# Optimization experiments

Measured on AMD Instinct MI355X. Metric: run time of the kernel, lower is better.

The kernel has to match this reference:

```python
import jax, jax.numpy as jnp
import numpy as np

PST_THD = 0.05
NMS_THD = 0.5
TOP_K = 1000  # max candidates kept before greedy NMS (fixed for jit)
IMG = 1024
NUM_CLASSES = 80


def _make_anchors(H, W):
    # Standard RetinaNet anchors: P3-P7, 3 ratios x 3 scales = 9 per location.
    levels = [3, 4, 5, 6, 7]
    ratios = np.array([0.5, 1.0, 2.0])
    scales = np.array([2 ** 0, 2 ** (1.0 / 3.0), 2 ** (2.0 / 3.0)])
    all_a = []
    for l in levels:
        stride = 2 ** l
        size = 2 ** (l + 2)
        base = []
        for r in ratios:
            for s in scales:
                area = (size * s) ** 2
                w = np.sqrt(area / r)
                h = w * r
                base.append([-w / 2, -h / 2, w / 2, h / 2])
        base = np.asarray(base)  # (9,4)
        fh, fw = H // stride, W // stride
        sx = (np.arange(fw) + 0.5) * stride
        sy = (np.arange(fh) + 0.5) * stride
        sxx, syy = np.meshgrid(sx, sy)
        shifts = np.stack([sxx.ravel(), syy.ravel(), sxx.ravel(), syy.ravel()], 1)
        all_a.append((shifts[:, None, :] + base[None, :, :]).reshape(-1, 4))
    return np.concatenate(all_a, 0).astype(np.float32)  # (A,4)


def setup_inputs() -> dict:
    key = jax.random.key(0)
    k1, k2 = jax.random.split(key)
    anchors = jnp.asarray(_make_anchors(IMG, IMG))  # (A,4)
    A = anchors.shape[0]
    classification = jax.random.uniform(k1, (1, A, NUM_CLASSES), dtype=jnp.float32)
    regression = jax.random.normal(k2, (1, A, 4), dtype=jnp.float32) * 0.5
    return {
        "classification": classification,
        "regression": regression,
        "anchors": anchors,
        "height": IMG,
        "width": IMG,
    }


def _postprocess(classification, regression, anchors, height, width):
    cls = classification[0]   # (A,C)
    reg = regression[0]       # (A,4)
    # --- BBoxTransform (std = [0.1,0.1,0.2,0.2]) ---
    wa = anchors[:, 2] - anchors[:, 0]
    ha = anchors[:, 3] - anchors[:, 1]
    cxa = anchors[:, 0] + 0.5 * wa
    cya = anchors[:, 1] + 0.5 * ha
    pcx = cxa + reg[:, 0] * 0.1 * wa
    pcy = cya + reg[:, 1] * 0.1 * ha
    pw = jnp.exp(reg[:, 2] * 0.2) * wa
    ph = jnp.exp(reg[:, 3] * 0.2) * ha
    # --- ClipBoxes ---
    x1 = jnp.clip(pcx - 0.5 * pw, 0.0, None)
    y1 = jnp.clip(pcy - 0.5 * ph, 0.0, None)
    x2 = jnp.minimum(pcx + 0.5 * pw, jnp.float32(width))
    y2 = jnp.minimum(pcy + 0.5 * ph, jnp.float32(height))
    boxes = jnp.stack([x1, y1, x2, y2], axis=1)  # (A,4)
    # --- score threshold + top-K candidate selection ---
    scores = jnp.max(cls, axis=1)
    class_id = jnp.argmax(cls, axis=1).astype(jnp.int32)
    masked = jnp.where(scores > PST_THD, scores, -1.0)
    top_s, idx = jax.lax.top_k(masked, TOP_K)  # sorted descending
    b = boxes[idx]                             # (K,4)
    c = class_id[idx]
    valid = top_s > PST_THD
    # --- greedy NMS over K candidates (classic py_cpu_nms, +1 areas) ---
    area = (b[:, 2] - b[:, 0] + 1.0) * (b[:, 3] - b[:, 1] + 1.0)
    xx1 = jnp.maximum(b[:, None, 0], b[None, :, 0])
    yy1 = jnp.maximum(b[:, None, 1], b[None, :, 1])
    xx2 = jnp.minimum(b[:, None, 2], b[None, :, 2])
    yy2 = jnp.minimum(b[:, None, 3], b[None, :, 3])
    inter = jnp.clip(xx2 - xx1 + 1.0, 0.0) * jnp.clip(yy2 - yy1 + 1.0, 0.0)
    iou = inter / (area[:, None] + area[None, :] - inter)  # (K,K)
    later = jnp.arange(TOP_K)

    def body(i, keep):
        supp = (iou[i] > NMS_THD) & (later > i) & keep[i]
        return keep & (~supp)

    keep = jax.lax.fori_loop(0, TOP_K, body, valid)
    nms_scores = jnp.where(keep, top_s, 0.0)
    nms_classes = jnp.where(keep, c, -1)
    nms_boxes = jnp.where(keep[:, None], b, 0.0)
    return nms_scores, nms_classes, nms_boxes


def reference(classification, regression, anchors, height, width):
    # Fixed-size padded equivalent of the original variable-length NMS output.
    return _postprocess(classification, regression, anchors, height, width)
```

## Files before the change

### kernel.cpp

```cpp
#include <hip/hip_runtime.h>
#include <stdint.h>

#define K_TOP 1000
#define PST 0.05f
#define THR 256
#define NTAIL 64

#define C_DONE0 0
#define C_BAR   4
#define C_BAR2  5
#define C_CNTA  6
#define C_CNTE  7
#define C_PREFIX 8
#define C_CUM    9

typedef unsigned long long ull;

__device__ __forceinline__ unsigned mapU(float f) {
  unsigned b = __float_as_uint(f);
  return (b & 0x80000000u) ? ~b : (b | 0x80000000u);
}
__device__ __forceinline__ float unmapU(unsigned u) {
  unsigned b = (u & 0x80000000u) ? (u ^ 0x80000000u) : ~u;
  return __uint_as_float(b);
}
__device__ __forceinline__ float scalar_dim(const int* p) {
  int v = *p;
  if (v > 0 && v < (1 << 20)) return (float)v;
  return __int_as_float(v);
}

__device__ __forceinline__ unsigned aldU(const unsigned* p) {
  return __hip_atomic_load(p, __ATOMIC_RELAXED, __HIP_MEMORY_SCOPE_AGENT);
}
__device__ __forceinline__ void astU(unsigned* p, unsigned v) {
  __hip_atomic_store(p, v, __ATOMIC_RELAXED, __HIP_MEMORY_SCOPE_AGENT);
}
__device__ __forceinline__ ull aldL(const ull* p) {
  return __hip_atomic_load(p, __ATOMIC_RELAXED, __HIP_MEMORY_SCOPE_AGENT);
}
__device__ __forceinline__ void astL(ull* p, ull v) {
  __hip_atomic_store(p, v, __ATOMIC_RELAXED, __HIP_MEMORY_SCOPE_AGENT);
}

__device__ __forceinline__ void gsync(unsigned* bar, unsigned target) {
  __syncthreads();
  if (threadIdx.x == 0) {
    __hip_atomic_fetch_add(bar, 1u, __ATOMIC_RELAXED, __HIP_MEMORY_SCOPE_AGENT);
    while (__hip_atomic_load(bar, __ATOMIC_RELAXED, __HIP_MEMORY_SCOPE_AGENT) < target)
      __builtin_amdgcn_s_sleep(1);
  }
  __syncthreads();
}

template <int NB>
__device__ void selectN(const unsigned* __restrict__ histL, int shift,
                        unsigned* __restrict__ ctrl) {
  constexpr int PB = NB / 64;
  int t = threadIdx.x;
  unsigned cumIn = ctrl[C_CUM];
  unsigned need = (unsigned)K_TOP - cumIn;
  unsigned h[PB];
  unsigned v = 0;
  #pragma unroll
  for (int b = 0; b < PB; ++b) { h[b] = histL[PB * t + b]; v += h[b]; }
  #pragma unroll
  for (int d = 1; d < 64; d <<= 1) {
    unsigned q = __shfl_down(v, d);
    if (t + d < 64) v += q;
  }
  unsigned sn = __shfl_down(v, 1);
  if (t == 63) sn = 0;
  if (v >= need && sn < need) {
    unsigned c = sn;
    int bsel = PB * t;
    for (int b = PB - 1; b >= 0; --b) {
      if (c + h[b] >= need) { bsel = PB * t + b; break; }
      c += h[b];
    }
    ctrl[C_PREFIX] = ctrl[C_PREFIX] | (((unsigned)bsel) << shift);
    ctrl[C_CUM] = cumIn + c;
  }
}

template <int NB>
__device__ void selectL(const unsigned* __restrict__ histL, int shift,
                        unsigned* sPref, unsigned* sCum) {
  constexpr int PB = NB / 64;
  int t = threadIdx.x;
  unsigned cumIn = *sCum;
  unsigned need = (unsigned)K_TOP - cumIn;
  unsigned h[PB];
  unsigned v = 0;
  #pragma unroll
  for (int b = 0; b < PB; ++b) { h[b] = aldU(&histL[PB * t + b]); v += h[b]; }
  #pragma unroll
  for (int d = 1; d < 64; d <<= 1) {
    unsigned q = __shfl_down(v, d);
    if (t + d < 64) v += q;
  }
  unsigned sn = __shfl_down(v, 1);
  if (t == 63) sn = 0;
  if (v >= need && sn < need) {
    unsigned c = sn;
    int bsel = PB * t;
    for (int b = PB - 1; b >= 0; --b) {
      if (c + h[b] >= need) { bsel = PB * t + b; break; }
      c += h[b];
    }
    *sPref = *sPref | (((unsigned)bsel) << shift);
    *sCum = cumIn + c;
  }
}

__global__ void __launch_bounds__(1024) k_init(unsigned* hist, unsigned* ctrl,
                                               ull* keyBuf, float* candS,
                                               int* candC, float4* candB) {
  int t = threadIdx.x;
  for (int e = t; e < 5120; e += 1024) hist[e] = 0u;
  if (t < 64) ctrl[t] = 0u;
  for (int e = t; e < 4096; e += 1024) keyBuf[e] = 0ull;
  candS[t] = -1.0f;
  candC[t] = -1;
  candB[t] = make_float4(0.f, 0.f, 0.f, 0.f);
}

__global__ void __launch_bounds__(THR) k_decode(
    const float* __restrict__ cls, const float* __restrict__ reg,
    const float* __restrict__ anc, const int* __restrict__ hp,
    const int* __restrict__ wp, int A, int C,
    float4* __restrict__ boxes, unsigned* __restrict__ su,
    int* __restrict__ ci, unsigned* hist0, unsigned* ctrl, int nb) {
  __shared__ unsigned lh[2048];
  int t = threadIdx.x;
  for (int b = t; b < 2048; b += THR) lh[b] = 0u;
  __syncthreads();
  int a = blockIdx.x * THR + t;
  if (a < A) {
    const float* row = cls + (size_t)a * C;
    float m = -3.4e38f; int mi = 0;
    int j = 0;
    for (; j + 4 <= C; j += 4) {
      float4 v = *(const float4*)(row + j);
      if (v.x > m) { m = v.x; mi = j; }
      if (v.y > m) { m = v.y; mi = j + 1; }
      if (v.z > m) { m = v.z; mi = j + 2; }
      if (v.w > m) { m = v.w; mi = j + 3; }
    }
    for (; j < C; ++j) { float v = row[j]; if (v > m) { m = v; mi = j; } }

    float4 an = ((const float4*)anc)[a];
    float4 rg = ((const float4*)reg)[a];
    float wa = an.z - an.x, ha = an.w - an.y;
    float cxa = an.x + 0.5f * wa, cya = an.y + 0.5f * ha;
    float pcx = cxa + rg.x * 0.1f * wa;
    float pcy = cya + rg.y * 0.1f * ha;
    float pw = expf(rg.z * 0.2f) * wa;
    float ph = expf(rg.w * 0.2f) * ha;
    float W = scalar_dim(wp), H = scalar_dim(hp);
    float x1 = fmaxf(pcx - 0.5f * pw, 0.f);
    float y1 = fmaxf(pcy - 0.5f * ph, 0.f);
    float x2 = fminf(pcx + 0.5f * pw, W);
    float y2 = fminf(pcy + 0.5f * ph, H);
    boxes[a] = make_float4(x1, y1, x2, y2);
    ci[a] = mi;
    float msk = (m > PST) ? m : -1.0f;
    unsigned u = mapU(msk);
    su[a] = u;
    atomicAdd(&lh[u >> 21], 1u);
  }
  __syncthreads();
  for (int b = t; b < 2048; b += THR)
    if (lh[b]) atomicAdd(&hist0[b], lh[b]);
  __shared__ int last;
  __syncthreads();
  if (t == 0) {
    unsigned old = __hip_atomic_fetch_add(&ctrl[C_DONE0], 1u,
                                          __ATOMIC_ACQ_REL, __HIP_MEMORY_SCOPE_AGENT);
    last = (old == (unsigned)(nb - 1));
  }
  __syncthreads();
  if (last && t < 64) selectN<2048>(hist0, 21, ctrl);
}

__global__ void __launch_bounds__(THR) k_sel(
    const unsigned* __restrict__ su, int A, ull* __restrict__ keyBuf,
    unsigned* hist, unsigned* ctrl) {
  __shared__ unsigned lh[2048];
  __shared__ unsigned sPref, sCum;
  int t = threadIdx.x;
  int g0 = blockIdx.x * THR + t;
  if (t == 0) { sPref = ctrl[C_PREFIX]; sCum = ctrl[C_CUM]; }

  for (int b = t; b < 2048; b += THR) lh[b] = 0u;
  __syncthreads();
  unsigned pref = sPref;
  for (int a = g0; a < A; a += NTAIL * THR) {
    unsigned u = su[a];
    if ((u & 0xFFE00000u) == pref) atomicAdd(&lh[(u >> 10) & 2047u], 1u);
  }
  __syncthreads();
  {
    int rot = (blockIdx.x * 331) & 2047;
    for (int k = 0; k < 2048; k += THR) {
      int b = (rot + k + t) & 2047;
      if (lh[b]) atomicAdd(&hist[2048 + b], lh[b]);
    }
  }
  gsync(&ctrl[C_BAR], NTAIL);
  if (t < 64) selectL<2048>(hist + 2048, 10, &sPref, &sCum);
  __syncthreads();

  for (int b = t; b < 1024; b += THR) lh[b] = 0u;
  __syncthreads();
  pref = sPref;
  for (int a = g0; a < A; a += NTAIL * THR) {
    unsigned u = su[a];
    if ((u & 0xFFFFFC00u) == pref) atomicAdd(&lh[u & 1023u], 1u);
  }
  __syncthreads();
  {
    int rot = (blockIdx.x * 331) & 1023;
    for (int k = 0; k < 1024; k += THR) {
      int b = (rot + k + t) & 1023;
      if (lh[b]) atomicAdd(&hist[4096 + b], lh[b]);
    }
  }
  gsync(&ctrl[C_BAR], 2 * NTAIL);
  if (t < 64) selectL<1024>(hist + 4096, 0, &sPref, &sCum);
  __syncthreads();
  unsigned uT = sPref;

  for (int a = g0; a < A; a += NTAIL * THR) {
    unsigned u = su[a];
    if (u > uT) {
      unsigned p = atomicAdd(&ctrl[C_CNTA], 1u);
      if (p < 1000u) astL(&keyBuf[p], (((ull)u) << 32) | (unsigned)(~a));
    } else if (u == uT) {
      unsigned p = atomicAdd(&ctrl[C_CNTE], 1u);
      if (p < 3072u) astL(&keyBuf[1024 + p], (((ull)u) << 32) | (unsigned)(~a));
    }
  }
}

__global__ void __launch_bounds__(THR) k_nmsall(
    const ull* __restrict__ keyBuf, const float4* __restrict__ boxes,
    const int* __restrict__ ci, int A, float* __restrict__ candS,
    int* __restrict__ candC, float4* __restrict__ candB,
    ull* __restrict__ maskBuf, unsigned* ctrl, float* __restrict__ out) {
  __shared__ ull shmem[2048];
  __shared__ ull keepW[16];
  __shared__ ull vbW[16];
  int t = threadIdx.x;

  unsigned nTop = aldU(&ctrl[C_CNTA]);
  unsigned nTie = aldU(&ctrl[C_CNTE]); if (nTie > 3072u) nTie = 3072u;
  for (int e = t; e < 1024; e += THR) shmem[e] = aldL(&keyBuf[e]);
  __syncthreads();
  int wid = t >> 6, lane = t & 63;
  int gw = blockIdx.x * 4 + wid;
  #pragma unroll
  for (int s2 = 0; s2 < 4; ++s2) {
    int sidx = gw * 4 + s2;
    ull k0 = shmem[sidx];
    if (k0 != 0ull) {
      unsigned cnt = 0;
      for (int e = lane; e < 1024; e += 64) cnt += (shmem[e] > k0) ? 1u : 0u;
      #pragma unroll
      for (int d = 32; d; d >>= 1) cnt += __shfl_down(cnt, d);
      if (lane == 0 && cnt < (unsigned)K_TOP) {
        unsigned idx = ~(unsigned)k0;
        float4 bb = boxes[idx];
        astU((unsigned*)&candS[cnt], __float_as_uint(unmapU((unsigned)(k0 >> 32))));
        astU((unsigned*)&candC[cnt], (unsigned)ci[idx]);
        ull* bp = (ull*)&candB[cnt];
        astL(bp, ((ull)__float_as_uint(bb.y) << 32) | __float_as_uint(bb.x));
        astL(bp + 1, ((ull)__float_as_uint(bb.w) << 32) | __float_as_uint(bb.z));
      }
    }
  }
  for (int tix = gw; tix < (int)nTie; tix += NTAIL * 4) {
    ull k0 = aldL(&keyBuf[1024 + tix]);
    unsigned cnt = 0;
    for (int e = lane; e < (int)nTie; e += 64)
      cnt += (aldL(&keyBuf[1024 + e]) > k0) ? 1u : 0u;
    #pragma unroll
    for (int d = 32; d; d >>= 1) cnt += __shfl_down(cnt, d);
    if (lane == 0) {
      unsigned rank = nTop + cnt;
      if (rank < (unsigned)K_TOP) {
        unsigned idx = ~(unsigned)k0;
        float4 bb = boxes[idx];
        astU((unsigned*)&candS[rank], __float_as_uint(unmapU((unsigned)(k0 >> 32))));
        astU((unsigned*)&candC[rank], (unsigned)ci[idx]);
        ull* bp = (ull*)&candB[rank];
        astL(bp, ((ull)__float_as_uint(bb.y) << 32) | __float_as_uint(bb.x));
        astL(bp + 1, ((ull)__float_as_uint(bb.w) << 32) | __float_as_uint(bb.z));
      }
    }
  }
  gsync(&ctrl[C_BAR2], NTAIL);

  float4* sCand = (float4*)shmem;
  for (int e = t; e < 1024; e += THR) {
    const ull* bp = (const ull*)&candB[e];
    ull lo = aldL(bp), hi = aldL(bp + 1);
    sCand[e] = make_float4(__uint_as_float((unsigned)lo),
                           __uint_as_float((unsigned)(lo >> 32)),
                           __uint_as_float((unsigned)hi),
                           __uint_as_float((unsigned)(hi >> 32)));
  }
  __syncthreads();
  {
    int g4 = blockIdx.x * THR + t;
    int i = g4 & 1023, w = g4 >> 10;
    float4 bi = sCand[i];
    float areai = (bi.z - bi.x + 1.f) * (bi.w - bi.y + 1.f);
    ull bits = 0ull;
    if (i < K_TOP) {
      int j0 = w << 6;
      #pragma unroll 4
      for (int b = 0; b < 64; ++b) {
        int j = j0 + b;
        if (j > i && j < K_TOP) {
          float4 bj = sCand[j];
          float xx1 = fmaxf(bi.x, bj.x);
          float yy1 = fmaxf(bi.y, bj.y);
          float xx2 = fminf(bi.z, bj.z);
          float yy2 = fminf(bi.w, bj.w);
          float iw = fmaxf(xx2 - xx1 + 1.f, 0.f);
          float ih = fmaxf(yy2 - yy1 + 1.f, 0.f);
          float inter = iw * ih;
          float areaj = (bj.z - bj.x + 1.f) * (bj.w - bj.y + 1.f);
          float iou = inter / (areai + areaj - inter);
          if (iou > 0.5f) bits |= (1ull << b);
        }
      }
    }
    astL(&maskBuf[i * 16 + w], bits);
  }
  gsync(&ctrl[C_BAR2], 2 * NTAIL);

  if (blockIdx.x != 0) return;
  ull (*buf)[1024] = (ull(*)[1024])shmem;
  __syncthreads();
  for (int q = t; q < 1024; q += THR) {
    float s = __uint_as_float(aldU((const unsigned*)&candS[q]));
    ull mball = __ballot(s > PST);
    if ((q & 63) == 0) vbW[q >> 6] = mball;
  }
  for (int e = t; e < 1024; e += THR) buf[0][e] = aldL(&maskBuf[e]);
  __syncthreads();

  ull remv = 0ull;
  int l = t & 63;
  if (t < 64 && l < 16) remv = ~vbW[l];
  for (int w = 0; w < 16; ++w) {
    if (w + 1 < 16 && t >= 64) {
      for (int e = t - 64; e < 1024; e += THR - 64)
        buf[(w + 1) & 1][e] = aldL(&maskBuf[(w + 1) * 1024 + e]);
    }
    if (t < 64) {
      ull cw = __shfl(remv, w);
      const ull* rows = buf[w & 1];
      #pragma unroll
      for (int b = 0; b < 64; ++b) {
        ull mrow = rows[b * 16 + (l & 15)];
        ull mvw  = rows[b * 16 + w];
        ull sel = ((cw >> b) & 1ull) - 1ull;
        remv |= (mrow & sel);
        cw   |= (mvw & sel);
      }
    }
    __syncthreads();
  }
  if (t < 64 && l < 16) keepW[l] = ~remv;
  __syncthreads();

  for (int q = t; q < K_TOP; q += THR) {
    bool kp = (keepW[q >> 6] >> (q & 63)) & 1ull;
    float sc = __uint_as_float(aldU((const unsigned*)&candS[q]));
    int cc = (int)aldU((const unsigned*)&candC[q]);
    const ull* bp = (const ull*)&candB[q];
    ull lo = aldL(bp), hi = aldL(bp + 1);
    out[q] = kp ? sc : 0.f;
    out[K_TOP + q] = kp ? (float)cc : -1.f;
    float4 ob = kp ? make_float4(__uint_as_float((unsigned)lo),
                                 __uint_as_float((unsigned)(lo >> 32)),
                                 __uint_as_float((unsigned)hi),
                                 __uint_as_float((unsigned)(hi >> 32)))
                   : make_float4(0.f, 0.f, 0.f, 0.f);
    *(float4*)(out + 2 * K_TOP + 4 * q) = ob;
  }
}

extern "C" void kernel_launch(void* const* d_in, const int* in_sizes, int n_in,
                              void* d_out, int out_size, void* d_ws, size_t ws_size,
                              hipStream_t stream) {
  const float* cls = (const float*)d_in[0];
  const float* reg = (const float*)d_in[1];
  const float* anc = (const float*)d_in[2];
  const int* hp = (const int*)d_in[3];
  const int* wp = (const int*)d_in[4];
  int A = in_sizes[2] / 4;
  int C = in_sizes[0] / A;

  char* ws = (char*)d_ws;
  size_t off = 0;
  auto alloc = [&](size_t bytes) -> void* {
    void* p = ws + off;
    off = (off + bytes + 255) & ~(size_t)255;
    return p;
  };
  float4* boxes = (float4*)alloc((size_t)A * 16);
  unsigned* su = (unsigned*)alloc((size_t)A * 4);
  int* ci = (int*)alloc((size_t)A * 4);
  ull* keyBuf = (ull*)alloc(4096 * 8);
  float* candS = (float*)alloc(1024 * 4);
  int* candC = (int*)alloc(1024 * 4);
  float4* candB = (float4*)alloc(1024 * 16);
  ull* maskBuf = (ull*)alloc(16384 * 8);
  unsigned* hist = (unsigned*)alloc(5120 * 4);
  unsigned* ctrl = (unsigned*)alloc(256 * 4);
  (void)ws_size; (void)n_in; (void)out_size;

  int nb = (A + THR - 1) / THR;

  hipLaunchKernelGGL(k_init, dim3(1), dim3(1024), 0, stream,
                     hist, ctrl, keyBuf, candS, candC, candB);
  hipLaunchKernelGGL(k_decode, dim3(nb), dim3(THR), 0, stream,
                     cls, reg, anc, hp, wp, A, C,
                     boxes, su, ci, hist, ctrl, nb);
  hipLaunchKernelGGL(k_sel, dim3(NTAIL), dim3(THR), 0, stream,
                     su, A, keyBuf, hist, ctrl);
  hipLaunchKernelGGL(k_nmsall, dim3(NTAIL), dim3(THR), 0, stream,
                     keyBuf, boxes, ci, A, candS, candC, candB,
                     maskBuf, ctrl, (float*)d_out);
}
```

Baseline: 223.5 us.

## Fuse selection and NMS kernels into one 1024-thread tail with 7-bit radix levels

Merges k_sel and k_nmsall into a single persistent k_tail kernel of 64 blocks with 1024 threads, chained by grid-wide barriers, which removes one kernel launch. The two refinement radix passes (11-bit then 10-bit) become three 7-bit passes using 128-bin histograms, so each histogram flush and select step is smaller but one more grid barrier is needed. Decode gets a specialised C==80 path that loads all 20 float4s up front and uses fmax reductions plus a min-index pass to find the argmax. The tradeoff is more global syncs and larger blocks in exchange for fewer launches and cheaper per-level work.

After: 206.6 us. 7.6% less time.

```diff
diff --git a/kernel.cpp b/kernel.cpp
--- a/kernel.cpp
+++ b/kernel.cpp
@@ -4,11 +4,11 @@
 #define K_TOP 1000
 #define PST 0.05f
 #define THR 256
+#define TTHR 1024
 #define NTAIL 64
 
 #define C_DONE0 0
 #define C_BAR   4
-#define C_BAR2  5
 #define C_CNTA  6
 #define C_CNTE  7
 #define C_PREFIX 8
@@ -117,7 +117,7 @@
                                                ull* keyBuf, float* candS,
                                                int* candC, float4* candB) {
   int t = threadIdx.x;
-  for (int e = t; e < 5120; e += 1024) hist[e] = 0u;
+  for (int e = t; e < 2560; e += 1024) hist[e] = 0u;
   if (t < 64) ctrl[t] = 0u;
   for (int e = t; e < 4096; e += 1024) keyBuf[e] = 0ull;
   candS[t] = -1.0f;
@@ -137,18 +137,33 @@
   __syncthreads();
   int a = blockIdx.x * THR + t;
   if (a < A) {
-    const float* row = cls + (size_t)a * C;
-    float m = -3.4e38f; int mi = 0;
-    int j = 0;
-    for (; j + 4 <= C; j += 4) {
-      float4 v = *(const float4*)(row + j);
-      if (v.x > m) { m = v.x; mi = j; }
-      if (v.y > m) { m = v.y; mi = j + 1; }
-      if (v.z > m) { m = v.z; mi = j + 2; }
-      if (v.w > m) { m = v.w; mi = j + 3; }
-    }
-    for (; j < C; ++j) { float v = row[j]; if (v > m) { m = v; mi = j; } }
-
+    float m; int mi;
+    if (C == 80) {
+      const float4* row = (const float4*)(cls + (size_t)a * 80);
+      float4 v[20];
+      #pragma unroll
+      for (int j = 0; j < 20; ++j) v[j] = row[j];
+      __builtin_amdgcn_sched_barrier(0);
+      float mx[20];
+      #pragma unroll
+      for (int j = 0; j < 20; ++j)
+        mx[j] = fmaxf(fmaxf(v[j].x, v[j].y), fmaxf(v[j].z, v[j].w));
+      m = mx[0];
+      #pragma unroll
+      for (int j = 1; j < 20; ++j) m = fmaxf(m, mx[j]);
+      mi = 0x7fffffff;
+      #pragma unroll
+      for (int j = 0; j < 20; ++j) {
+        mi = min(mi, (v[j].x == m) ? 4 * j + 0 : 0x7fffffff);
+        mi = min(mi, (v[j].y == m) ? 4 * j + 1 : 0x7fffffff);
+        mi = min(mi, (v[j].z == m) ? 4 * j + 2 : 0x7fffffff);
+        mi = min(mi, (v[j].w == m) ? 4 * j + 3 : 0x7fffffff);
+      }
+    } else {
+      const float* row = cls + (size_t)a * C;
+      m = -3.4e38f; mi = 0;
+      for (int j = 0; j < C; ++j) { float v = row[j]; if (v > m) { m = v; mi = j; } }
+    }
     float4 an = ((const float4*)anc)[a];
     float4 rg = ((const float4*)reg)[a];
     float wa = an.z - an.x, ha = an.w - an.y;
@@ -183,55 +198,42 @@
   if (last && t < 64) selectN<2048>(hist0, 21, ctrl);
 }
 
-__global__ void __launch_bounds__(THR) k_sel(
-    const unsigned* __restrict__ su, int A, ull* __restrict__ keyBuf,
-    unsigned* hist, unsigned* ctrl) {
-  __shared__ unsigned lh[2048];
+__global__ void __launch_bounds__(TTHR) k_tail(
+    const unsigned* __restrict__ su, int A,
+    const float4* __restrict__ boxes, const int* __restrict__ ci,
+    ull* __restrict__ keyBuf, float* __restrict__ candS,
+    int* __restrict__ candC, float4* __restrict__ candB,
+    ull* __restrict__ maskBuf, unsigned* hist, unsigned* ctrl,
+    float* __restrict__ out) {
+  __shared__ ull shmem[2048];
+  __shared__ ull keepW[16];
+  __shared__ ull vbW[16];
+  __shared__ unsigned lh[128];
   __shared__ unsigned sPref, sCum;
   int t = threadIdx.x;
-  int g0 = blockIdx.x * THR + t;
   if (t == 0) { sPref = ctrl[C_PREFIX]; sCum = ctrl[C_CUM]; }
 
-  for (int b = t; b < 2048; b += THR) lh[b] = 0u;
-  __syncthreads();
-  unsigned pref = sPref;
-  for (int a = g0; a < A; a += NTAIL * THR) {
-    unsigned u = su[a];
-    if ((u & 0xFFE00000u) == pref) atomicAdd(&lh[(u >> 10) & 2047u], 1u);
-  }
-  __syncthreads();
-  {
-    int rot = (blockIdx.x * 331) & 2047;
-    for (int k = 0; k < 2048; k += THR) {
-      int b = (rot + k + t) & 2047;
-      if (lh[b]) atomicAdd(&hist[2048 + b], lh[b]);
-    }
-  }
-  gsync(&ctrl[C_BAR], NTAIL);
-  if (t < 64) selectL<2048>(hist + 2048, 10, &sPref, &sCum);
-  __syncthreads();
-
-  for (int b = t; b < 1024; b += THR) lh[b] = 0u;
-  __syncthreads();
-  pref = sPref;
-  for (int a = g0; a < A; a += NTAIL * THR) {
-    unsigned u = su[a];
-    if ((u & 0xFFFFFC00u) == pref) atomicAdd(&lh[u & 1023u], 1u);
-  }
-  __syncthreads();
-  {
-    int rot = (blockIdx.x * 331) & 1023;
-    for (int k = 0; k < 1024; k += THR) {
-      int b = (rot + k + t) & 1023;
-      if (lh[b]) atomicAdd(&hist[4096 + b], lh[b]);
-    }
-  }
-  gsync(&ctrl[C_BAR], 2 * NTAIL);
-  if (t < 64) selectL<1024>(hist + 4096, 0, &sPref, &sCum);
-  __syncthreads();
+  #pragma unroll
+  for (int lev = 0; lev < 3; ++lev) {
+    const int shift = 14 - 7 * lev;
+    const unsigned pm = 0xFFFFFFFFu << (shift + 7);
+    unsigned* hl = hist + 2048 + 128 * lev;
+    if (t < 128) lh[t] = 0u;
+    __syncthreads();
+    unsigned pref = sPref;
+    for (int a = blockIdx.x * TTHR + t; a < A; a += NTAIL * TTHR) {
+      unsigned u = su[a];
+      if ((u & pm) == pref) atomicAdd(&lh[(u >> shift) & 127u], 1u);
+    }
+    __syncthreads();
+    if (t < 128 && lh[t]) atomicAdd(&hl[t], lh[t]);
+    gsync(&ctrl[C_BAR], (lev + 1) * NTAIL);
+    if (t < 64) selectL<128>(hl, shift, &sPref, &sCum);
+    __syncthreads();
+  }
   unsigned uT = sPref;
 
-  for (int a = g0; a < A; a += NTAIL * THR) {
+  for (int a = blockIdx.x * TTHR + t; a < A; a += NTAIL * TTHR) {
     unsigned u = su[a];
     if (u > uT) {
       unsigned p = atomicAdd(&ctrl[C_CNTA], 1u);
@@ -241,28 +243,16 @@
       if (p < 3072u) astL(&keyBuf[1024 + p], (((ull)u) << 32) | (unsigned)(~a));
     }
   }
-}
-
-__global__ void __launch_bounds__(THR) k_nmsall(
-    const ull* __restrict__ keyBuf, const float4* __restrict__ boxes,
-    const int* __restrict__ ci, int A, float* __restrict__ candS,
-    int* __restrict__ candC, float4* __restrict__ candB,
-    ull* __restrict__ maskBuf, unsigned* ctrl, float* __restrict__ out) {
-  __shared__ ull shmem[2048];
-  __shared__ ull keepW[16];
-  __shared__ ull vbW[16];
-  int t = threadIdx.x;
+  gsync(&ctrl[C_BAR], 4 * NTAIL);
 
   unsigned nTop = aldU(&ctrl[C_CNTA]);
   unsigned nTie = aldU(&ctrl[C_CNTE]); if (nTie > 3072u) nTie = 3072u;
-  for (int e = t; e < 1024; e += THR) shmem[e] = aldL(&keyBuf[e]);
+  if (t < 1024) shmem[t] = aldL(&keyBuf[t]);
   __syncthreads();
   int wid = t >> 6, lane = t & 63;
-  int gw = blockIdx.x * 4 + wid;
-  #pragma unroll
-  for (int s2 = 0; s2 < 4; ++s2) {
-    int sidx = gw * 4 + s2;
-    ull k0 = shmem[sidx];
+  int gw = blockIdx.x * 16 + wid;
+  {
+    ull k0 = shmem[gw];
     if (k0 != 0ull) {
       unsigned cnt = 0;
       for (int e = lane; e < 1024; e += 64) cnt += (shmem[e] > k0) ? 1u : 0u;
@@ -279,7 +269,7 @@
       }
     }
   }
-  for (int tix = gw; tix < (int)nTie; tix += NTAIL * 4) {
+  for (int tix = gw; tix < (int)nTie; tix += NTAIL * 16) {
     ull k0 = aldL(&keyBuf[1024 + tix]);
     unsigned cnt = 0;
     for (int e = lane; e < (int)nTie; e += 64)
@@ -299,10 +289,10 @@
       }
     }
   }
-  gsync(&ctrl[C_BAR2], NTAIL);
+  gsync(&ctrl[C_BAR], 5 * NTAIL);
 
   float4* sCand = (float4*)shmem;
-  for (int e = t; e < 1024; e += THR) {
+  for (int e = t; e < 1024; e += TTHR) {
     const ull* bp = (const ull*)&candB[e];
     ull lo = aldL(bp), hi = aldL(bp + 1);
     sCand[e] = make_float4(__uint_as_float((unsigned)lo),
@@ -311,9 +301,8 @@
                            __uint_as_float((unsigned)(hi >> 32)));
   }
   __syncthreads();
-  {
-    int g4 = blockIdx.x * THR + t;
-    int i = g4 & 1023, w = g4 >> 10;
+  if (blockIdx.x < 16) {
+    int i = t, w = blockIdx.x;
     float4 bi = sCand[i];
     float areai = (bi.z - bi.x + 1.f) * (bi.w - bi.y + 1.f);
     ull bits = 0ull;
@@ -339,17 +328,17 @@
     }
     astL(&maskBuf[i * 16 + w], bits);
   }
-  gsync(&ctrl[C_BAR2], 2 * NTAIL);
+  gsync(&ctrl[C_BAR], 6 * NTAIL);
 
   if (blockIdx.x != 0) return;
   ull (*buf)[1024] = (ull(*)[1024])shmem;
   __syncthreads();
-  for (int q = t; q < 1024; q += THR) {
-    float s = __uint_as_float(aldU((const unsigned*)&candS[q]));
+  if (t < 1024) {
+    float s = __uint_as_float(aldU((const unsigned*)&candS[t]));
     ull mball = __ballot(s > PST);
-    if ((q & 63) == 0) vbW[q >> 6] = mball;
-  }
-  for (int e = t; e < 1024; e += THR) buf[0][e] = aldL(&maskBuf[e]);
+    if ((t & 63) == 0) vbW[t >> 6] = mball;
+  }
+  if (t < 1024) buf[0][t] = aldL(&maskBuf[t]);
   __syncthreads();
 
   ull remv = 0ull;
@@ -357,7 +346,7 @@
   if (t < 64 && l < 16) remv = ~vbW[l];
   for (int w = 0; w < 16; ++w) {
     if (w + 1 < 16 && t >= 64) {
-      for (int e = t - 64; e < 1024; e += THR - 64)
+      for (int e = t - 64; e < 1024; e += TTHR - 64)
         buf[(w + 1) & 1][e] = aldL(&maskBuf[(w + 1) * 1024 + e]);
     }
     if (t < 64) {
@@ -377,7 +366,7 @@
   if (t < 64 && l < 16) keepW[l] = ~remv;
   __syncthreads();
 
-  for (int q = t; q < K_TOP; q += THR) {
+  for (int q = t; q < K_TOP; q += TTHR) {
     bool kp = (keepW[q >> 6] >> (q & 63)) & 1ull;
     float sc = __uint_as_float(aldU((const unsigned*)&candS[q]));
     int cc = (int)aldU((const unsigned*)&candC[q]);
@@ -420,7 +409,7 @@
   int* candC = (int*)alloc(1024 * 4);
   float4* candB = (float4*)alloc(1024 * 16);
   ull* maskBuf = (ull*)alloc(16384 * 8);
-  unsigned* hist = (unsigned*)alloc(5120 * 4);
+  unsigned* hist = (unsigned*)alloc(2560 * 4);
   unsigned* ctrl = (unsigned*)alloc(256 * 4);
   (void)ws_size; (void)n_in; (void)out_size;
 
@@ -431,9 +420,7 @@
   hipLaunchKernelGGL(k_decode, dim3(nb), dim3(THR), 0, stream,
                      cls, reg, anc, hp, wp, A, C,
                      boxes, su, ci, hist, ctrl, nb);
-  hipLaunchKernelGGL(k_sel, dim3(NTAIL), dim3(THR), 0, stream,
-                     su, A, keyBuf, hist, ctrl);
-  hipLaunchKernelGGL(k_nmsall, dim3(NTAIL), dim3(THR), 0, stream,
-                     keyBuf, boxes, ci, A, candS, candC, candB,
-                     maskBuf, ctrl, (float*)d_out);
-}
+  hipLaunchKernelGGL(k_tail, dim3(NTAIL), dim3(TTHR), 0, stream,
+                     su, A, boxes, ci, keyBuf, candS, candC, candB,
+                     maskBuf, hist, ctrl, (float*)d_out);
+}
```
